# Kernel tuning notes

Hardware: AMD Instinct MI355X
Metric: run time of the kernel (lower is better)

## Reference

```python
import jax, jax.numpy as jnp
import numpy as np

T, B = 2048, 64
E, H = 256, 256
VOCAB = 50257
PAD_ID = 0


def setup_inputs() -> dict:
    key = jax.random.key(0)
    ks = jax.random.split(key, 9)
    s = 0.05
    return {
        "sentences": jax.random.randint(ks[0], (T, B), 0, VOCAB, dtype=jnp.int64 if jax.config.jax_enable_x64 else jnp.int32),
        "noise": jax.random.uniform(ks[1], (T, B), dtype=jnp.float32),
        "emb": jax.random.normal(ks[2], (VOCAB, E), dtype=jnp.float32) * s,
        "W_ih": jax.random.normal(ks[3], (4 * H, E), dtype=jnp.float32) * s,
        "W_hh": jax.random.normal(ks[4], (4 * H, H), dtype=jnp.float32) * s,
        "b_ih": jax.random.normal(ks[5], (4 * H,), dtype=jnp.float32) * s,
        "b_hh": jax.random.normal(ks[6], (4 * H,), dtype=jnp.float32) * s,
        "W_z": jax.random.normal(ks[7], (H,), dtype=jnp.float32) * s,
        "b_z": jax.random.normal(ks[8], (), dtype=jnp.float32) * s,
    }


def _lstm(x, W_ih, W_hh, b_ih, b_hh):
    # x: (T, B, E) -> hidden states (T, B, H). PyTorch gate order: i, f, g, o.
    Hd = W_hh.shape[1]
    h0 = jnp.zeros((x.shape[1], Hd), x.dtype)
    c0 = jnp.zeros((x.shape[1], Hd), x.dtype)
    b = b_ih + b_hh

    def step(carry, x_t):
        h, c = carry
        g = x_t @ W_ih.T + h @ W_hh.T + b  # (B, 4H)
        i, f, gg, o = jnp.split(g, 4, axis=-1)
        c = jax.nn.sigmoid(f) * c + jax.nn.sigmoid(i) * jnp.tanh(gg)
        h = jax.nn.sigmoid(o) * jnp.tanh(c)
        return (h, c), h

    _, hs = jax.lax.scan(step, (h0, c0), x)
    return hs


def reference(sentences, noise, emb, W_ih, W_hh, b_ih, b_hh, W_z, b_z):
    x = emb[sentences]                         # (T, B, E) embedding gather
    hs = _lstm(x, W_ih, W_hh, b_ih, b_hh)      # (T, B, H)
    pz = jax.nn.sigmoid(jnp.einsum("tbh,h->tb", hs, W_z) + b_z)  # (T, B)
    z = (noise < pz).astype(pz.dtype)          # Bernoulli sample via uniform noise
    z_sizes = z.sum(axis=0).astype(jnp.int32)  # (B,)
    # Stream compaction per column: stable sort brings z==1 positions first,
    # preserving original token order (parallel equivalent of masked_select loop).
    order = jnp.argsort((1.0 - z).astype(jnp.int32), axis=0, stable=True)  # (T, B)
    selected = jnp.take_along_axis(sentences, order.astype(sentences.dtype), axis=0)
    pos = jnp.arange(sentences.shape[0])[:, None]
    rationales = jnp.where(pos < z_sizes[None, :], selected,
                           jnp.asarray(PAD_ID, sentences.dtype))
    return (pz, z, rationales, z_sizes)
```

## Files before the change

kernel.cpp:

```cpp
#include <hip/hip_runtime.h>
#include <math.h>

#define TT 2048
#define NB 64
#define EE 256
#define HH 256
#define PJ 16
#define XLD 288
#define RS1 280
#define RS2 72
#define RBOFF (8 * RS1)

typedef float f32x4 __attribute__((ext_vector_type(4)));

__device__ __forceinline__ float sigf(float x) { return 1.f / (1.f + expf(-x)); }

__device__ __forceinline__ unsigned long long packh(unsigned tag, float v) {
    union { float f; unsigned u; } c; c.f = v;
    return ((unsigned long long)tag << 32) | (unsigned long long)c.u;
}

__global__ __launch_bounds__(512, 2)
void lstm_kernel(const int* __restrict__ sent, const float* __restrict__ emb,
                 const float* __restrict__ W_ih, const float* __restrict__ W_hh,
                 const float* __restrict__ b_ih, const float* __restrict__ b_hh,
                 const float* __restrict__ W_z,
                 unsigned long long* __restrict__ hbuf,
                 float* __restrict__ part)
{
    __shared__ float x_sw[4 * XLD];
    __shared__ float h_sw[4 * XLD];
    __shared__ float red_s[2 * 8 * RS1];
    __shared__ float p_s[64];
    extern __shared__ float dyn_pad[];

    const int tid  = threadIdx.x;
    if (tid == 0 && sent[0] < 0) ((volatile float*)dyn_pad)[0] = 0.f;

    const int xcd  = blockIdx.x & 7;
    const int slot = blockIdx.x >> 3;
    const int psys = xcd * 2 + (slot >> 4);
    const int js   = slot & 15;
    const int bA0  = psys * 2;
    const int bB0  = 32 + psys * 2;
    const int j0   = js * 16;

    const int wv    = tid >> 6;
    const int lane  = tid & 63;
    const int bp    = wv & 1;
    const int kc    = (wv >> 1) * 2 + (lane & 1);
    const int rg    = lane >> 1;
    const int kbase = kc << 5;

    float4 wih_r[16], whh_r[16];
    #pragma unroll
    for (int i = 0; i < 2; ++i) {
        int lr = rg * 2 + i;
        long grow = (long)((lr >> 4) * HH + j0 + (lr & 15));
        const float4* wi = (const float4*)(W_ih + grow * EE + kbase);
        const float4* wh = (const float4*)(W_hh + grow * EE + kbase);
        #pragma unroll
        for (int mi = 0; mi < 8; ++mi) {
            wih_r[i * 8 + mi] = wi[mi];
            whh_r[i * 8 + mi] = wh[mi];
        }
    }

    const int eb  = (lane >> 4) & 1;
    const int ejj = lane & 15;
    float bias_g[4]; float wz_r = 0.f; float c_reg = 0.f;
    if (wv < 2) {
        #pragma unroll
        for (int g = 0; g < 4; ++g)
            bias_g[g] = b_ih[g * HH + j0 + ejj] + b_hh[g * HH + j0 + ejj];
        wz_r = W_z[j0 + ejj];
    }

    const bool inA = (wv >= 2 && wv <= 4) || wv == 7;
    const bool inB = (wv >= 4);
    const int aidx = ((wv == 7 ? 3 : wv - 2) << 6) + lane;
    const int bidx = ((wv - 4) << 6) + lane;
    const int acb = aidx >> 7, acw = (aidx & 127) << 1;
    const int bcb = bidx >> 7, bcw = (bidx & 127) << 1;
    const int acph = acw + ((acw >> 5) << 2);
    const int bcph = bcw + ((bcw >> 5) << 2);

    const int stb   = wv & 1;
    const int stRow = (wv >= 6 ? 2 : 0) + stb;
    const int sphys = 4 * lane + ((lane >> 3) << 2);
    int tok_st = 0;

    if (wv >= 4) {
        int base = (wv >= 6) ? bB0 : bA0;
        int tk0 = sent[0 * NB + base + stb];
        f32x4 xv0 = ((const f32x4*)(emb + (long)tk0 * EE))[lane];
        *(f32x4*)(&x_sw[stRow * XLD + sphys]) = xv0;
        tok_st = sent[1 * NB + base + stb];
    }
    __syncthreads();

    for (int t = 0; t < TT; ++t) {
        const bool pf = (t + 1 < TT);
        const size_t parIn  = (size_t)(((t - 1) & 1) * NB);
        const size_t parOut = (size_t)((t & 1) * NB);

        f32x4 xst;
        if (pf && wv == 5) {
            xst = ((const f32x4*)(emb + (long)tok_st * EE))[lane];
            if (t + 2 < TT) tok_st = sent[(t + 2) * NB + bA0 + stb];
        }

        float4 acc[2];
        acc[0] = make_float4(0.f, 0.f, 0.f, 0.f);
        acc[1] = make_float4(0.f, 0.f, 0.f, 0.f);
        {
            const float* xb = &x_sw[bp * XLD + kc * 36];
            #pragma unroll
            for (int mi = 0; mi < 8; ++mi) {
                float4 xv4 = *(const float4*)(xb + mi * 4);
                #pragma unroll
                for (int i = 0; i < 2; ++i) {
                    float4 w = wih_r[i * 8 + mi];
                    acc[i].x += w.x * xv4.x; acc[i].y += w.y * xv4.y;
                    acc[i].z += w.z * xv4.z; acc[i].w += w.w * xv4.w;
                }
            }
        }
        if (t > 0 && inA) {
            const unsigned want = (unsigned)t;
            unsigned long long* hp =
                hbuf + (parIn + bA0 + acb) * HH + acw;
            unsigned long long v0, v1;
            v0 = __hip_atomic_load(hp + 0, __ATOMIC_RELAXED, __HIP_MEMORY_SCOPE_AGENT);
            v1 = __hip_atomic_load(hp + 1, __ATOMIC_RELAXED, __HIP_MEMORY_SCOPE_AGENT);
            while ((unsigned)(v0 >> 32) != want)
                v0 = __hip_atomic_load(hp + 0, __ATOMIC_RELAXED, __HIP_MEMORY_SCOPE_AGENT);
            while ((unsigned)(v1 >> 32) != want)
                v1 = __hip_atomic_load(hp + 1, __ATOMIC_RELAXED, __HIP_MEMORY_SCOPE_AGENT);
            union { unsigned u; float f; } c0, c1;
            c0.u = (unsigned)v0; c1.u = (unsigned)v1;
            *(float2*)(&h_sw[acb * XLD + acph]) = make_float2(c0.f, c1.f);
        }
        if (pf && wv == 4) {
            xst = ((const f32x4*)(emb + (long)tok_st * EE))[lane];
            if (t + 2 < TT) tok_st = sent[(t + 2) * NB + bA0 + stb];
        }
        __syncthreads();

        if (t > 0 && wv == 2 && lane < 2) {
            float s = 0.f;
            #pragma unroll
            for (int jj = 0; jj < 16; ++jj) s += p_s[lane * 16 + jj];
            part[((size_t)(t - 1) * PJ + js) * NB + bA0 + lane] = s;
        }
        if (t > 0) {
            const float* hb = &h_sw[bp * XLD + kc * 36];
            #pragma unroll
            for (int mi = 0; mi < 8; ++mi) {
                float4 hv4 = *(const float4*)(hb + mi * 4);
                #pragma unroll
                for (int i = 0; i < 2; ++i) {
                    float4 w = whh_r[i * 8 + mi];
                    acc[i].x += w.x * hv4.x; acc[i].y += w.y * hv4.y;
                    acc[i].z += w.z * hv4.z; acc[i].w += w.w * hv4.w;
                }
            }
        }
        {
            float2 v;
            v.x = (acc[0].x + acc[0].y) + (acc[0].z + acc[0].w);
            v.y = (acc[1].x + acc[1].y) + (acc[1].z + acc[1].w);
            *(float2*)(&red_s[kc * RS1 + bp * RS2 + rg * 2]) = v;
        }
        if (pf && (wv == 4 || wv == 5)) {
            *(f32x4*)(&x_sw[stRow * XLD + sphys]) = xst;
        }
        __syncthreads();

        if (wv == 0 && lane < 32) {
            float sg[4];
            #pragma unroll
            for (int g = 0; g < 4; ++g) {
                float s = bias_g[g];
                #pragma unroll
                for (int k2 = 0; k2 < 8; ++k2)
                    s += red_s[k2 * RS1 + eb * RS2 + g * 16 + ejj];
                sg[g] = s;
            }
            float cn = sigf(sg[1]) * c_reg + sigf(sg[0]) * tanhf(sg[2]);
            float hn = sigf(sg[3]) * tanhf(cn);
            c_reg = cn;
            p_s[lane] = hn * wz_r;
            __hip_atomic_store(
                hbuf + (parOut + bA0 + eb) * HH + j0 + ejj,
                packh((unsigned)(t + 1), hn),
                __ATOMIC_RELAXED, __HIP_MEMORY_SCOPE_AGENT);
        }

        acc[0] = make_float4(0.f, 0.f, 0.f, 0.f);
        acc[1] = make_float4(0.f, 0.f, 0.f, 0.f);
        {
            const float* xb = &x_sw[(2 + bp) * XLD + kc * 36];
            #pragma unroll
            for (int mi = 0; mi < 8; ++mi) {
                float4 xv4 = *(const float4*)(xb + mi * 4);
                #pragma unroll
                for (int i = 0; i < 2; ++i) {
                    float4 w = wih_r[i * 8 + mi];
                    acc[i].x += w.x * xv4.x; acc[i].y += w.y * xv4.y;
                    acc[i].z += w.z * xv4.z; acc[i].w += w.w * xv4.w;
                }
            }
        }
        if (t > 0 && inB) {
            const unsigned want = (unsigned)t;
            unsigned long long* hp =
                hbuf + (parIn + bB0 + bcb) * HH + bcw;
            unsigned long long v0, v1;
            v0 = __hip_atomic_load(hp + 0, __ATOMIC_RELAXED, __HIP_MEMORY_SCOPE_AGENT);
            v1 = __hip_atomic_load(hp + 1, __ATOMIC_RELAXED, __HIP_MEMORY_SCOPE_AGENT);
            while ((unsigned)(v0 >> 32) != want)
                v0 = __hip_atomic_load(hp + 0, __ATOMIC_RELAXED, __HIP_MEMORY_SCOPE_AGENT);
            while ((unsigned)(v1 >> 32) != want)
                v1 = __hip_atomic_load(hp + 1, __ATOMIC_RELAXED, __HIP_MEMORY_SCOPE_AGENT);
            union { unsigned u; float f; } c0, c1;
            c0.u = (unsigned)v0; c1.u = (unsigned)v1;
            *(float2*)(&h_sw[(2 + bcb) * XLD + bcph]) = make_float2(c0.f, c1.f);
        }
        if (pf && (wv == 6 || wv == 7)) {
            xst = ((const f32x4*)(emb + (long)tok_st * EE))[lane];
            if (t + 2 < TT) tok_st = sent[(t + 2) * NB + bB0 + stb];
        }
        __syncthreads();

        if (t > 0 && wv == 3 && lane < 2) {
            float s = 0.f;
            #pragma unroll
            for (int jj = 0; jj < 16; ++jj) s += p_s[32 + lane * 16 + jj];
            part[((size_t)(t - 1) * PJ + js) * NB + bB0 + lane] = s;
        }
        if (t > 0) {
            const float* hb = &h_sw[(2 + bp) * XLD + kc * 36];
            #pragma unroll
            for (int mi = 0; mi < 8; ++mi) {
                float4 hv4 = *(const float4*)(hb + mi * 4);
                #pragma unroll
                for (int i = 0; i < 2; ++i) {
                    float4 w = whh_r[i * 8 + mi];
                    acc[i].x += w.x * hv4.x; acc[i].y += w.y * hv4.y;
                    acc[i].z += w.z * hv4.z; acc[i].w += w.w * hv4.w;
                }
            }
        }
        {
            float2 v;
            v.x = (acc[0].x + acc[0].y) + (acc[0].z + acc[0].w);
            v.y = (acc[1].x + acc[1].y) + (acc[1].z + acc[1].w);
            *(float2*)(&red_s[RBOFF + kc * RS1 + bp * RS2 + rg * 2]) = v;
        }
        if (pf && (wv == 6 || wv == 7)) {
            *(f32x4*)(&x_sw[stRow * XLD + sphys]) = xst;
        }
        __syncthreads();

        if (wv == 1 && lane < 32) {
            float sg[4];
            #pragma unroll
            for (int g = 0; g < 4; ++g) {
                float s = bias_g[g];
                #pragma unroll
                for (int k2 = 0; k2 < 8; ++k2)
                    s += red_s[RBOFF + k2 * RS1 + eb * RS2 + g * 16 + ejj];
                sg[g] = s;
            }
            float cn = sigf(sg[1]) * c_reg + sigf(sg[0]) * tanhf(sg[2]);
            float hn = sigf(sg[3]) * tanhf(cn);
            c_reg = cn;
            p_s[32 + lane] = hn * wz_r;
            __hip_atomic_store(
                hbuf + (parOut + bB0 + eb) * HH + j0 + ejj,
                packh((unsigned)(t + 1), hn),
                __ATOMIC_RELAXED, __HIP_MEMORY_SCOPE_AGENT);
        }
    }

    __syncthreads();
    if (wv == 2 && lane < 2) {
        float s = 0.f;
        #pragma unroll
        for (int jj = 0; jj < 16; ++jj) s += p_s[lane * 16 + jj];
        part[((size_t)(TT - 1) * PJ + js) * NB + bA0 + lane] = s;
    }
    if (wv == 3 && lane < 2) {
        float s = 0.f;
        #pragma unroll
        for (int jj = 0; jj < 16; ++jj) s += p_s[32 + lane * 16 + jj];
        part[((size_t)(TT - 1) * PJ + js) * NB + bB0 + lane] = s;
    }
}

__global__ void pz_kernel(const float* __restrict__ part,
                          const float* __restrict__ noise,
                          const float* __restrict__ b_z,
                          float* __restrict__ out)
{
    int idx = blockIdx.x * blockDim.x + threadIdx.x;
    if (idx >= TT * NB) return;
    int t = idx >> 6, b = idx & 63;
    float s = b_z[0];
    #pragma unroll
    for (int jg = 0; jg < PJ; ++jg) s += part[(t * PJ + jg) * NB + b];
    float pz = 1.f / (1.f + expf(-s));
    out[idx] = pz;
    out[TT * NB + idx] = (noise[idx] < pz) ? 1.f : 0.f;
}

__global__ void compact_kernel(const int* __restrict__ sent,
                               const float* __restrict__ zbuf,
                               float* __restrict__ rat,
                               float* __restrict__ zsz)
{
    __shared__ float rat_s[TT];
    __shared__ int scan_s[256];
    int b = blockIdx.x, tid = threadIdx.x;
    int zloc[8];
    int base = tid * 8;
    int c = 0;
    #pragma unroll
    for (int i = 0; i < 8; ++i) {
        zloc[i] = (zbuf[(base + i) * NB + b] != 0.f) ? 1 : 0;
        c += zloc[i];
    }
    scan_s[tid] = c;
    for (int i = tid; i < TT; i += 256) rat_s[i] = 0.f;
    __syncthreads();
    for (int off = 1; off < 256; off <<= 1) {
        int v = scan_s[tid];
        int add = (tid >= off) ? scan_s[tid - off] : 0;
        __syncthreads();
        scan_s[tid] = v + add;
        __syncthreads();
    }
    int total = scan_s[255];
    int pos = scan_s[tid] - c;
    #pragma unroll
    for (int i = 0; i < 8; ++i) {
        if (zloc[i]) { rat_s[pos] = (float)sent[(base + i) * NB + b]; ++pos; }
    }
    __syncthreads();
    for (int i = tid; i < TT; i += 256) rat[i * NB + b] = rat_s[i];
    if (tid == 0) zsz[b] = (float)total;
}

extern "C" void kernel_launch(void* const* d_in, const int* in_sizes, int n_in,
                              void* d_out, int out_size, void* d_ws, size_t ws_size,
                              hipStream_t stream)
{
    const int*   sent  = (const int*)d_in[0];
    const float* noise = (const float*)d_in[1];
    const float* emb   = (const float*)d_in[2];
    const float* W_ih  = (const float*)d_in[3];
    const float* W_hh  = (const float*)d_in[4];
    const float* b_ih  = (const float*)d_in[5];
    const float* b_hh  = (const float*)d_in[6];
    const float* W_z   = (const float*)d_in[7];
    const float* b_z   = (const float*)d_in[8];
    float* out = (float*)d_out;

    char* ws = (char*)d_ws;
    unsigned long long* hbuf = (unsigned long long*)ws;
    float* part = (float*)(ws + 262144);

    (void)hipMemsetAsync(hbuf, 0, 2 * NB * HH * sizeof(unsigned long long), stream);

    lstm_kernel<<<256, 512, 65536, stream>>>(sent, emb, W_ih, W_hh, b_ih, b_hh,
                                             W_z, hbuf, part);
    pz_kernel<<<(TT * NB) / 256, 256, 0, stream>>>(part, noise, b_z, out);
    compact_kernel<<<NB, 256, 0, stream>>>(sent, out + TT * NB,
                                           out + 2 * TT * NB, out + 3 * TT * NB);
}
```

Measured before the change: 4.360 ms.

## Issue h polling loads early, rebalance wave roles, vectorize gate reduction reads

The first probe of the cross-block hidden-state flags is now issued before the x-projection FMA loop, so global-load latency overlaps with compute rather than sitting after it. Wave roles are reshuffled: waves 0-3 now handle embedding prefetch, A-half polling moves to waves 2-5, and waves 4-7 poll the B half, with some B loads hoisted into the A phase. The reduction scratch is transposed so each gate thread reads its four gate partials with one 16-byte LDS load instead of four scalar loads. In exchange, the partial-sum writes become two scalar stores, the wave roles couple more tightly, and early loads that fail must still go through the spin loop.

```diff
diff --git a/kernel.cpp b/kernel.cpp
--- a/kernel.cpp
+++ b/kernel.cpp
@@ -28,10 +28,10 @@
                  unsigned long long* __restrict__ hbuf,
                  float* __restrict__ part)
 {
-    __shared__ float x_sw[4 * XLD];
-    __shared__ float h_sw[4 * XLD];
-    __shared__ float red_s[2 * 8 * RS1];
-    __shared__ float p_s[64];
+    __shared__ __align__(16) float x_sw[4 * XLD];
+    __shared__ __align__(16) float h_sw[4 * XLD];
+    __shared__ __align__(16) float red_s[2 * 8 * RS1];
+    __shared__ __align__(16) float p_s[64];
     extern __shared__ float dyn_pad[];
 
     const int tid  = threadIdx.x;
@@ -66,6 +66,8 @@
         }
     }
 
+    const int p0 = ((rg * 2) & 15) * 4 + ((rg * 2) >> 4);
+
     const int eb  = (lane >> 4) & 1;
     const int ejj = lane & 15;
     float bias_g[4]; float wz_r = 0.f; float c_reg = 0.f;
@@ -76,26 +78,24 @@
         wz_r = W_z[j0 + ejj];
     }
 
-    const bool inA = (wv >= 2 && wv <= 4) || wv == 7;
+    const bool inA = (wv >= 2 && wv <= 5);
     const bool inB = (wv >= 4);
-    const int aidx = ((wv == 7 ? 3 : wv - 2) << 6) + lane;
-    const int bidx = ((wv - 4) << 6) + lane;
+    const int aidx = (((wv - 2) & 3) << 6) + lane;
+    const int bidx = (((wv - 4) & 3) << 6) + lane;
     const int acb = aidx >> 7, acw = (aidx & 127) << 1;
     const int bcb = bidx >> 7, bcw = (bidx & 127) << 1;
     const int acph = acw + ((acw >> 5) << 2);
     const int bcph = bcw + ((bcw >> 5) << 2);
 
-    const int stb   = wv & 1;
-    const int stRow = (wv >= 6 ? 2 : 0) + stb;
     const int sphys = 4 * lane + ((lane >> 3) << 2);
     int tok_st = 0;
 
-    if (wv >= 4) {
-        int base = (wv >= 6) ? bB0 : bA0;
-        int tk0 = sent[0 * NB + base + stb];
+    if (wv < 4) {
+        int base = (wv < 2) ? bA0 : bB0;
+        int tk0 = sent[0 * NB + base + bp];
         f32x4 xv0 = ((const f32x4*)(emb + (long)tk0 * EE))[lane];
-        *(f32x4*)(&x_sw[stRow * XLD + sphys]) = xv0;
-        tok_st = sent[1 * NB + base + stb];
+        *(f32x4*)(&x_sw[wv * XLD + sphys]) = xv0;
+        tok_st = sent[1 * NB + base + bp];
     }
     __syncthreads();
 
@@ -103,11 +103,23 @@
         const bool pf = (t + 1 < TT);
         const size_t parIn  = (size_t)(((t - 1) & 1) * NB);
         const size_t parOut = (size_t)((t & 1) * NB);
+        const unsigned want = (unsigned)t;
 
         f32x4 xst;
-        if (pf && wv == 5) {
+        if (pf && wv < 2) {
             xst = ((const f32x4*)(emb + (long)tok_st * EE))[lane];
-            if (t + 2 < TT) tok_st = sent[(t + 2) * NB + bA0 + stb];
+            if (t + 2 < TT) tok_st = sent[(t + 2) * NB + bA0 + bp];
+        }
+        unsigned long long a0 = 0, a1 = 0, b0v = 0, b1v = 0;
+        unsigned long long* hpA = hbuf + (parIn + bA0 + acb) * HH + acw;
+        unsigned long long* hpB = hbuf + (parIn + bB0 + bcb) * HH + bcw;
+        if (t > 0 && inA) {
+            a0 = __hip_atomic_load(hpA + 0, __ATOMIC_RELAXED, __HIP_MEMORY_SCOPE_AGENT);
+            a1 = __hip_atomic_load(hpA + 1, __ATOMIC_RELAXED, __HIP_MEMORY_SCOPE_AGENT);
+        }
+        if (t > 0 && wv >= 6) {
+            b0v = __hip_atomic_load(hpB + 0, __ATOMIC_RELAXED, __HIP_MEMORY_SCOPE_AGENT);
+            b1v = __hip_atomic_load(hpB + 1, __ATOMIC_RELAXED, __HIP_MEMORY_SCOPE_AGENT);
         }
 
         float4 acc[2];
@@ -127,23 +139,21 @@
             }
         }
         if (t > 0 && inA) {
-            const unsigned want = (unsigned)t;
-            unsigned long long* hp =
-                hbuf + (parIn + bA0 + acb) * HH + acw;
-            unsigned long long v0, v1;
-            v0 = __hip_atomic_load(hp + 0, __ATOMIC_RELAXED, __HIP_MEMORY_SCOPE_AGENT);
-            v1 = __hip_atomic_load(hp + 1, __ATOMIC_RELAXED, __HIP_MEMORY_SCOPE_AGENT);
-            while ((unsigned)(v0 >> 32) != want)
-                v0 = __hip_atomic_load(hp + 0, __ATOMIC_RELAXED, __HIP_MEMORY_SCOPE_AGENT);
-            while ((unsigned)(v1 >> 32) != want)
-                v1 = __hip_atomic_load(hp + 1, __ATOMIC_RELAXED, __HIP_MEMORY_SCOPE_AGENT);
+            while ((unsigned)(a0 >> 32) != want)
+                a0 = __hip_atomic_load(hpA + 0, __ATOMIC_RELAXED, __HIP_MEMORY_SCOPE_AGENT);
+            while ((unsigned)(a1 >> 32) != want)
+                a1 = __hip_atomic_load(hpA + 1, __ATOMIC_RELAXED, __HIP_MEMORY_SCOPE_AGENT);
             union { unsigned u; float f; } c0, c1;
-            c0.u = (unsigned)v0; c1.u = (unsigned)v1;
+            c0.u = (unsigned)a0; c1.u = (unsigned)a1;
             *(float2*)(&h_sw[acb * XLD + acph]) = make_float2(c0.f, c1.f);
         }
-        if (pf && wv == 4) {
+        if (pf && (wv == 2 || wv == 3)) {
             xst = ((const f32x4*)(emb + (long)tok_st * EE))[lane];
-            if (t + 2 < TT) tok_st = sent[(t + 2) * NB + bA0 + stb];
+            if (t + 2 < TT) tok_st = sent[(t + 2) * NB + bB0 + bp];
+        }
+        if (t > 0 && (wv == 4 || wv == 5)) {
+            b0v = __hip_atomic_load(hpB + 0, __ATOMIC_RELAXED, __HIP_MEMORY_SCOPE_AGENT);
+            b1v = __hip_atomic_load(hpB + 1, __ATOMIC_RELAXED, __HIP_MEMORY_SCOPE_AGENT);
         }
         __syncthreads();
 
@@ -167,28 +177,25 @@
             }
         }
         {
-            float2 v;
-            v.x = (acc[0].x + acc[0].y) + (acc[0].z + acc[0].w);
-            v.y = (acc[1].x + acc[1].y) + (acc[1].z + acc[1].w);
-            *(float2*)(&red_s[kc * RS1 + bp * RS2 + rg * 2]) = v;
-        }
-        if (pf && (wv == 4 || wv == 5)) {
-            *(f32x4*)(&x_sw[stRow * XLD + sphys]) = xst;
+            float vx = (acc[0].x + acc[0].y) + (acc[0].z + acc[0].w);
+            float vy = (acc[1].x + acc[1].y) + (acc[1].z + acc[1].w);
+            red_s[kc * RS1 + bp * RS2 + p0]     = vx;
+            red_s[kc * RS1 + bp * RS2 + p0 + 4] = vy;
+        }
+        if (pf && wv < 2) {
+            *(f32x4*)(&x_sw[wv * XLD + sphys]) = xst;
         }
         __syncthreads();
 
         if (wv == 0 && lane < 32) {
-            float sg[4];
-            #pragma unroll
-            for (int g = 0; g < 4; ++g) {
-                float s = bias_g[g];
-                #pragma unroll
-                for (int k2 = 0; k2 < 8; ++k2)
-                    s += red_s[k2 * RS1 + eb * RS2 + g * 16 + ejj];
-                sg[g] = s;
-            }
-            float cn = sigf(sg[1]) * c_reg + sigf(sg[0]) * tanhf(sg[2]);
-            float hn = sigf(sg[3]) * tanhf(cn);
+            float sg0 = bias_g[0], sg1 = bias_g[1], sg2 = bias_g[2], sg3 = bias_g[3];
+            #pragma unroll
+            for (int k2 = 0; k2 < 8; ++k2) {
+                f32x4 rv = *(const f32x4*)(&red_s[k2 * RS1 + eb * RS2 + ejj * 4]);
+                sg0 += rv.x; sg1 += rv.y; sg2 += rv.z; sg3 += rv.w;
+            }
+            float cn = sigf(sg1) * c_reg + sigf(sg0) * tanhf(sg2);
+            float hn = sigf(sg3) * tanhf(cn);
             c_reg = cn;
             p_s[lane] = hn * wz_r;
             __hip_atomic_store(
@@ -213,23 +220,13 @@
             }
         }
         if (t > 0 && inB) {
-            const unsigned want = (unsigned)t;
-            unsigned long long* hp =
-                hbuf + (parIn + bB0 + bcb) * HH + bcw;
-            unsigned long long v0, v1;
-            v0 = __hip_atomic_load(hp + 0, __ATOMIC_RELAXED, __HIP_MEMORY_SCOPE_AGENT);
-            v1 = __hip_atomic_load(hp + 1, __ATOMIC_RELAXED, __HIP_MEMORY_SCOPE_AGENT);
-            while ((unsigned)(v0 >> 32) != want)
-                v0 = __hip_atomic_load(hp + 0, __ATOMIC_RELAXED, __HIP_MEMORY_SCOPE_AGENT);
-            while ((unsigned)(v1 >> 32) != want)
-                v1 = __hip_atomic_load(hp + 1, __ATOMIC_RELAXED, __HIP_MEMORY_SCOPE_AGENT);
+            while ((unsigned)(b0v >> 32) != want)
+                b0v = __hip_atomic_load(hpB + 0, __ATOMIC_RELAXED, __HIP_MEMORY_SCOPE_AGENT);
+            while ((unsigned)(b1v >> 32) != want)
+                b1v = __hip_atomic_load(hpB + 1, __ATOMIC_RELAXED, __HIP_MEMORY_SCOPE_AGENT);
             union { unsigned u; float f; } c0, c1;
-            c0.u = (unsigned)v0; c1.u = (unsigned)v1;
+            c0.u = (unsigned)b0v; c1.u = (unsigned)b1v;
             *(float2*)(&h_sw[(2 + bcb) * XLD + bcph]) = make_float2(c0.f, c1.f);
-        }
-        if (pf && (wv == 6 || wv == 7)) {
-            xst = ((const f32x4*)(emb + (long)tok_st * EE))[lane];
-            if (t + 2 < TT) tok_st = sent[(t + 2) * NB + bB0 + stb];
         }
         __syncthreads();
 
@@ -253,28 +250,25 @@
             }
         }
         {
-            float2 v;
-            v.x = (acc[0].x + acc[0].y) + (acc[0].z + acc[0].w);
-            v.y = (acc[1].x + acc[1].y) + (acc[1].z + acc[1].w);
-            *(float2*)(&red_s[RBOFF + kc * RS1 + bp * RS2 + rg * 2]) = v;
-        }
-        if (pf && (wv == 6 || wv == 7)) {
-            *(f32x4*)(&x_sw[stRow * XLD + sphys]) = xst;
+            float vx = (acc[0].x + acc[0].y) + (acc[0].z + acc[0].w);
+            float vy = (acc[1].x + acc[1].y) + (acc[1].z + acc[1].w);
+            red_s[RBOFF + kc * RS1 + bp * RS2 + p0]     = vx;
+            red_s[RBOFF + kc * RS1 + bp * RS2 + p0 + 4] = vy;
+        }
+        if (pf && (wv == 2 || wv == 3)) {
+            *(f32x4*)(&x_sw[wv * XLD + sphys]) = xst;
         }
         __syncthreads();
 
         if (wv == 1 && lane < 32) {
-            float sg[4];
-            #pragma unroll
-            for (int g = 0; g < 4; ++g) {
-                float s = bias_g[g];
-                #pragma unroll
-                for (int k2 = 0; k2 < 8; ++k2)
-                    s += red_s[RBOFF + k2 * RS1 + eb * RS2 + g * 16 + ejj];
-                sg[g] = s;
-            }
-            float cn = sigf(sg[1]) * c_reg + sigf(sg[0]) * tanhf(sg[2]);
-            float hn = sigf(sg[3]) * tanhf(cn);
+            float sg0 = bias_g[0], sg1 = bias_g[1], sg2 = bias_g[2], sg3 = bias_g[3];
+            #pragma unroll
+            for (int k2 = 0; k2 < 8; ++k2) {
+                f32x4 rv = *(const f32x4*)(&red_s[RBOFF + k2 * RS1 + eb * RS2 + ejj * 4]);
+                sg0 += rv.x; sg1 += rv.y; sg2 += rv.z; sg3 += rv.w;
+            }
+            float cn = sigf(sg1) * c_reg + sigf(sg0) * tanhf(sg2);
+            float hn = sigf(sg3) * tanhf(cn);
             c_reg = cn;
             p_s[32 + lane] = hn * wz_r;
             __hip_atomic_store(
```

Result: slower. 4.964 ms (+13.9%).
